# Performance work log

Measured on AMD Instinct MI355X. Metric: run time of the kernel, lower is better.

## Reference

```python
import jax, jax.numpy as jnp
import numpy as np

MPPI_ITER = 6
HORIZON = 18
NUM_SAMPLES = 65536
ACTION_DIM = 4
NUM_ELITES = 64
STD = 0.5
MOMENTUM = 0.1
TEMPERATURE = 1.0


def setup_inputs() -> dict:
    key = jax.random.key(0)
    k1, k2, k3 = jax.random.split(key, 3)
    pi_actions = jax.random.normal(k1, (HORIZON, NUM_SAMPLES, ACTION_DIM), dtype=jnp.float32)
    noise = jax.random.normal(k2, (MPPI_ITER, HORIZON, NUM_SAMPLES, ACTION_DIM), dtype=jnp.float32)
    target = jax.random.normal(k3, (HORIZON, ACTION_DIM), dtype=jnp.float32)
    return {"pi_actions": pi_actions, "noise": noise, "target": target}


def _value(actions, target):
    # Surrogate for methods.estimate_value: quadratic trajectory cost.
    # actions: [H, N, A], target: [H, A] -> value: [N]
    return -jnp.sum((actions - target[:, None, :]) ** 2, axis=(0, 2))


def reference(pi_actions, noise, target):
    H, N, A = pi_actions.shape
    mean = pi_actions[:, 0, :]                      # [H, A]
    std = jnp.ones((H, A), dtype=pi_actions.dtype)  # [H, A]
    elite_actions = pi_actions[:, :NUM_ELITES, :]
    for i in range(MPPI_ITER):
        # sample CEM trajectories around (mean, std), clamp to action bounds
        cem_actions = jnp.clip(
            mean[:, None, :] + STD * std[:, None, :] * noise[i], -4.0, 4.0
        )                                                      # [H, N, A]
        actions = jnp.concatenate([pi_actions, cem_actions], axis=1)  # [H, 2N, A]
        value = _value(actions, target)                        # [2N]
        elite_value, elite_idxs = jax.lax.top_k(value, NUM_ELITES)    # [E]
        elite_actions = actions[:, elite_idxs, :]              # [H, E, A]
        # exp-weighted reweighting (faithful double normalization of `score`)
        max_value = jnp.max(elite_value)
        score = jnp.exp(TEMPERATURE * (elite_value - max_value))
        score = score / jnp.sum(score)
        ssum = jnp.sum(score)
        _mean = jnp.sum(score[None, :, None] * elite_actions, axis=1) / (ssum + 1e-9)
        _std = jnp.sqrt(
            jnp.sum(score[None, :, None] * (elite_actions - _mean[:, None, :]) ** 2, axis=1)
            / (ssum + 1e-9)
        )
        # faithful reproduction of clamp_(horizon, 2): min=18 > max=2 -> pins to 2
        _std = jnp.clip(_std, float(H), 2.0)
        mean = MOMENTUM * mean + (1.0 - MOMENTUM) * _mean
        std = _std
    a = elite_actions[:, 0, :]  # best elite action sequence [H, A]
    return a
```

## Files before the change

### kernel.cpp

```cpp
#include <hip/hip_runtime.h>
#include <math.h>

#define H 18
#define NS 65536
#define AD 4
#define HAD 72
#define ITERS 6
#define DELTA 16.0f
#define SCAP 2048
#define NCH 2048

__device__ __forceinline__ unsigned encf(float f) {
    unsigned u = __float_as_uint(f);
    return (u & 0x80000000u) ? ~u : (u | 0x80000000u);
}
__device__ __forceinline__ float decf(unsigned u) {
    return __uint_as_float((u & 0x80000000u) ? (u & 0x7FFFFFFFu) : ~u);
}
__device__ __forceinline__ float clamp4f(float x) { return fminf(fmaxf(x, -4.0f), 4.0f); }
__device__ __forceinline__ unsigned long long packkey(float v, unsigned idx) {
    return ((unsigned long long)encf(v) << 32) | (unsigned long long)(~idx);
}

#define QH0(q) ((q) == 0 ? 0 : (q) == 1 ? 5 : (q) == 2 ? 10 : 14)
#define QCN(q) ((q) < 2 ? 5 : 4)

__global__ void __launch_bounds__(256, 4) k_value0(
        const float4* __restrict__ pi4, const float4* __restrict__ nz4,
        const float* __restrict__ target, float* __restrict__ meanarr,
        float* __restrict__ v_pi, float* __restrict__ wmax_pi,
        float* __restrict__ v_c0, float* __restrict__ wmax_c0) {
    __shared__ float tgt[HAD], mnL[HAD];
    __shared__ float smaxc[4], smaxp[4];
    const int tid = threadIdx.x, wg = blockIdx.x;
    const int lane = tid & 63, wid = tid >> 6;
    const int q = lane >> 4, s = lane & 15;
    const int n = wg * 64 + wid * 16 + s;
    const int h0 = QH0(q), cnt = QCN(q);

    float4 xs0 = nz4[(size_t)(h0 + 0) * NS + n];
    float4 xs1 = nz4[(size_t)(h0 + 1) * NS + n];
    float4 xs2 = nz4[(size_t)(h0 + 2) * NS + n];
    float4 xs3 = nz4[(size_t)(h0 + 3) * NS + n];
    const int h4 = (h0 + 4 > 17) ? 17 : h0 + 4;
    float4 xs4 = nz4[(size_t)h4 * NS + n];
    float4 ps0 = pi4[(size_t)(h0 + 0) * NS + n];
    float4 ps1 = pi4[(size_t)(h0 + 1) * NS + n];
    float4 ps2 = pi4[(size_t)(h0 + 2) * NS + n];
    float4 ps3 = pi4[(size_t)(h0 + 3) * NS + n];
    float4 ps4 = pi4[(size_t)h4 * NS + n];

    if (tid < HAD) {
        tgt[tid] = target[tid];
        float m0 = ((const float*)pi4)[(size_t)(tid >> 2) * NS * AD + (tid & 3)];
        mnL[tid] = m0;
        meanarr[tid] = m0;
    }
    __syncthreads();

    const float w4 = (cnt == 5) ? 1.0f : 0.0f;
    float a2 = 0.f, p2 = 0.f;
    {
        float c; int h;
        h = h0 + 0;
        c = clamp4f(mnL[h*4+0] + 0.5f*xs0.x) - tgt[h*4+0]; a2 += c*c;
        c = clamp4f(mnL[h*4+1] + 0.5f*xs0.y) - tgt[h*4+1]; a2 += c*c;
        c = clamp4f(mnL[h*4+2] + 0.5f*xs0.z) - tgt[h*4+2]; a2 += c*c;
        c = clamp4f(mnL[h*4+3] + 0.5f*xs0.w) - tgt[h*4+3]; a2 += c*c;
        c = ps0.x - tgt[h*4+0]; p2 += c*c;  c = ps0.y - tgt[h*4+1]; p2 += c*c;
        c = ps0.z - tgt[h*4+2]; p2 += c*c;  c = ps0.w - tgt[h*4+3]; p2 += c*c;
        h = h0 + 1;
        c = clamp4f(mnL[h*4+0] + 0.5f*xs1.x) - tgt[h*4+0]; a2 += c*c;
        c = clamp4f(mnL[h*4+1] + 0.5f*xs1.y) - tgt[h*4+1]; a2 += c*c;
        c = clamp4f(mnL[h*4+2] + 0.5f*xs1.z) - tgt[h*4+2]; a2 += c*c;
        c = clamp4f(mnL[h*4+3] + 0.5f*xs1.w) - tgt[h*4+3]; a2 += c*c;
        c = ps1.x - tgt[h*4+0]; p2 += c*c;  c = ps1.y - tgt[h*4+1]; p2 += c*c;
        c = ps1.z - tgt[h*4+2]; p2 += c*c;  c = ps1.w - tgt[h*4+3]; p2 += c*c;
        h = h0 + 2;
        c = clamp4f(mnL[h*4+0] + 0.5f*xs2.x) - tgt[h*4+0]; a2 += c*c;
        c = clamp4f(mnL[h*4+1] + 0.5f*xs2.y) - tgt[h*4+1]; a2 += c*c;
        c = clamp4f(mnL[h*4+2] + 0.5f*xs2.z) - tgt[h*4+2]; a2 += c*c;
        c = clamp4f(mnL[h*4+3] + 0.5f*xs2.w) - tgt[h*4+3]; a2 += c*c;
        c = ps2.x - tgt[h*4+0]; p2 += c*c;  c = ps2.y - tgt[h*4+1]; p2 += c*c;
        c = ps2.z - tgt[h*4+2]; p2 += c*c;  c = ps2.w - tgt[h*4+3]; p2 += c*c;
        h = h0 + 3;
        c = clamp4f(mnL[h*4+0] + 0.5f*xs3.x) - tgt[h*4+0]; a2 += c*c;
        c = clamp4f(mnL[h*4+1] + 0.5f*xs3.y) - tgt[h*4+1]; a2 += c*c;
        c = clamp4f(mnL[h*4+2] + 0.5f*xs3.z) - tgt[h*4+2]; a2 += c*c;
        c = clamp4f(mnL[h*4+3] + 0.5f*xs3.w) - tgt[h*4+3]; a2 += c*c;
        c = ps3.x - tgt[h*4+0]; p2 += c*c;  c = ps3.y - tgt[h*4+1]; p2 += c*c;
        c = ps3.z - tgt[h*4+2]; p2 += c*c;  c = ps3.w - tgt[h*4+3]; p2 += c*c;
        h = h4;
        c = clamp4f(mnL[h*4+0] + 0.5f*xs4.x) - tgt[h*4+0]; a2 += w4*c*c;
        c = clamp4f(mnL[h*4+1] + 0.5f*xs4.y) - tgt[h*4+1]; a2 += w4*c*c;
        c = clamp4f(mnL[h*4+2] + 0.5f*xs4.z) - tgt[h*4+2]; a2 += w4*c*c;
        c = clamp4f(mnL[h*4+3] + 0.5f*xs4.w) - tgt[h*4+3]; a2 += w4*c*c;
        c = ps4.x - tgt[h*4+0]; p2 += w4*c*c;  c = ps4.y - tgt[h*4+1]; p2 += w4*c*c;
        c = ps4.z - tgt[h*4+2]; p2 += w4*c*c;  c = ps4.w - tgt[h*4+3]; p2 += w4*c*c;
    }
    a2 += __shfl_xor(a2, 16);  a2 += __shfl_xor(a2, 32);
    p2 += __shfl_xor(p2, 16);  p2 += __shfl_xor(p2, 32);
    const float vc = -a2, vp = -p2;
    if (lane < 16) { v_c0[n] = vc; v_pi[n] = vp; }
    float mc = vc, mp = vp;
#pragma unroll
    for (int off = 8; off; off >>= 1) {
        mc = fmaxf(mc, __shfl_xor(mc, off));
        mp = fmaxf(mp, __shfl_xor(mp, off));
    }
    if (lane == 0) { smaxc[wid] = mc; smaxp[wid] = mp; }
    __syncthreads();
    if (tid == 0) {
        wmax_c0[wg * 2 + 0] = fmaxf(smaxc[0], smaxc[1]);
        wmax_c0[wg * 2 + 1] = fmaxf(smaxc[2], smaxc[3]);
        wmax_pi[wg * 2 + 0] = fmaxf(smaxp[0], smaxp[1]);
        wmax_pi[wg * 2 + 1] = fmaxf(smaxp[2], smaxp[3]);
    }
}

__global__ void __launch_bounds__(256, 4) k_value(
        const float4* __restrict__ nz4, const float* __restrict__ target,
        const float* __restrict__ meanarr_i,
        float* __restrict__ v_out, float* __restrict__ wmax_out) {
    __shared__ float tgt[HAD], mnL[HAD];
    __shared__ float smax[4];
    const int tid = threadIdx.x, wg = blockIdx.x;
    const int lane = tid & 63, wid = tid >> 6;
    const int q = lane >> 4, s = lane & 15;
    const int n = wg * 64 + wid * 16 + s;
    const int h0 = QH0(q), cnt = QCN(q);

    float4 xs0 = nz4[(size_t)(h0 + 0) * NS + n];
    float4 xs1 = nz4[(size_t)(h0 + 1) * NS + n];
    float4 xs2 = nz4[(size_t)(h0 + 2) * NS + n];
    float4 xs3 = nz4[(size_t)(h0 + 3) * NS + n];
    const int h4 = (h0 + 4 > 17) ? 17 : h0 + 4;
    float4 xs4 = nz4[(size_t)h4 * NS + n];

    if (tid < HAD) { tgt[tid] = target[tid]; mnL[tid] = meanarr_i[tid]; }
    __syncthreads();

    const float w4 = (cnt == 5) ? 1.0f : 0.0f;
    float a2 = 0.f;
    {
        float c; int h;
        h = h0 + 0;
        c = clamp4f(mnL[h*4+0] + xs0.x) - tgt[h*4+0]; a2 += c*c;
        c = clamp4f(mnL[h*4+1] + xs0.y) - tgt[h*4+1]; a2 += c*c;
        c = clamp4f(mnL[h*4+2] + xs0.z) - tgt[h*4+2]; a2 += c*c;
        c = clamp4f(mnL[h*4+3] + xs0.w) - tgt[h*4+3]; a2 += c*c;
        h = h0 + 1;
        c = clamp4f(mnL[h*4+0] + xs1.x) - tgt[h*4+0]; a2 += c*c;
        c = clamp4f(mnL[h*4+1] + xs1.y) - tgt[h*4+1]; a2 += c*c;
        c = clamp4f(mnL[h*4+2] + xs1.z) - tgt[h*4+2]; a2 += c*c;
        c = clamp4f(mnL[h*4+3] + xs1.w) - tgt[h*4+3]; a2 += c*c;
        h = h0 + 2;
        c = clamp4f(mnL[h*4+0] + xs2.x) - tgt[h*4+0]; a2 += c*c;
        c = clamp4f(mnL[h*4+1] + xs2.y) - tgt[h*4+1]; a2 += c*c;
        c = clamp4f(mnL[h*4+2] + xs2.z) - tgt[h*4+2]; a2 += c*c;
        c = clamp4f(mnL[h*4+3] + xs2.w) - tgt[h*4+3]; a2 += c*c;
        h = h0 + 3;
        c = clamp4f(mnL[h*4+0] + xs3.x) - tgt[h*4+0]; a2 += c*c;
        c = clamp4f(mnL[h*4+1] + xs3.y) - tgt[h*4+1]; a2 += c*c;
        c = clamp4f(mnL[h*4+2] + xs3.z) - tgt[h*4+2]; a2 += c*c;
        c = clamp4f(mnL[h*4+3] + xs3.w) - tgt[h*4+3]; a2 += c*c;
        h = h4;
        c = clamp4f(mnL[h*4+0] + xs4.x) - tgt[h*4+0]; a2 += w4*c*c;
        c = clamp4f(mnL[h*4+1] + xs4.y) - tgt[h*4+1]; a2 += w4*c*c;
        c = clamp4f(mnL[h*4+2] + xs4.z) - tgt[h*4+2]; a2 += w4*c*c;
        c = clamp4f(mnL[h*4+3] + xs4.w) - tgt[h*4+3]; a2 += w4*c*c;
    }
    a2 += __shfl_xor(a2, 16);  a2 += __shfl_xor(a2, 32);
    const float vc = -a2;
    if (lane < 16) v_out[n] = vc;
    float m = vc;
#pragma unroll
    for (int off = 8; off; off >>= 1) m = fmaxf(m, __shfl_xor(m, off));
    if (lane == 0) smax[wid] = m;
    __syncthreads();
    if (tid == 0) {
        wmax_out[wg * 2 + 0] = fmaxf(smax[0], smax[1]);
        wmax_out[wg * 2 + 1] = fmaxf(smax[2], smax[3]);
    }
}

__global__ void __launch_bounds__(1024) k_reduce(
        const float* __restrict__ pi, const float* __restrict__ noise_i,
        float* __restrict__ meanarr,
        const float* __restrict__ wmax_pi, const float* __restrict__ v_pi,
        const float* __restrict__ wmax_c, const float* __restrict__ v_c,
        float* __restrict__ out, int iter, int is_last) {
    __shared__ unsigned long long skey[SCAP];
    __shared__ unsigned long long top[64];
    __shared__ unsigned long long redk[16];
    __shared__ float buf[64 * 76];
    __shared__ float w64[64];
    __shared__ float mprev[HAD];
    __shared__ float redf[16];
    __shared__ unsigned s_fcnt;
    __shared__ float s_S, s_gmax;
    const int tid = threadIdx.x, lane = tid & 63, wid = tid >> 6;

    if (tid < HAD) mprev[tid] = meanarr[iter * HAD + tid];
    if (tid == 0) s_fcnt = 0u;
    __syncthreads();

    {
        float g = fmaxf(fmaxf(wmax_pi[tid], wmax_pi[tid + 1024]),
                        fmaxf(wmax_c[tid], wmax_c[tid + 1024]));
        for (int off = 32; off; off >>= 1) g = fmaxf(g, __shfl_xor(g, off));
        if (lane == 0) redf[wid] = g;
        __syncthreads();
        if (tid == 0) {
            float x = redf[0];
            for (int q = 1; q < 16; ++q) x = fmaxf(x, redf[q]);
            s_gmax = x;
        }
        __syncthreads();
    }
    const float gmax = s_gmax, thr = gmax - DELTA;

#pragma unroll
    for (int r = 0; r < 2; ++r) {
        const int c = tid + r * 1024;
        if (wmax_pi[c] >= thr) {
            const float4* v4 = (const float4*)v_pi + c * 8;
            for (int q = 0; q < 8; ++q) {
                float4 x = v4[q];
                float vv[4] = {x.x, x.y, x.z, x.w};
#pragma unroll
                for (int c2 = 0; c2 < 4; ++c2)
                    if (vv[c2] >= thr) {
                        unsigned p = atomicAdd(&s_fcnt, 1u);
                        if (p < SCAP) skey[p] = packkey(vv[c2], (unsigned)(c * 32 + q * 4 + c2));
                    }
            }
        }
        if (wmax_c[c] >= thr) {
            const float4* v4 = (const float4*)v_c + c * 8;
            for (int q = 0; q < 8; ++q) {
                float4 x = v4[q];
                float vv[4] = {x.x, x.y, x.z, x.w};
#pragma unroll
                for (int c2 = 0; c2 < 4; ++c2)
                    if (vv[c2] >= thr) {
                        unsigned p = atomicAdd(&s_fcnt, 1u);
                        if (p < SCAP) skey[p] = packkey(vv[c2], (unsigned)(NS + c * 32 + q * 4 + c2));
                    }
            }
        }
    }
    __syncthreads();
    unsigned fc = s_fcnt; if (fc > SCAP) fc = SCAP;
    const float pscale = (iter == 0) ? 0.5f : 1.0f;

    if (is_last) {
        unsigned long long bk = 0ull;
        for (unsigned k = tid; k < fc; k += 1024) if (skey[k] > bk) bk = skey[k];
        for (int off = 32; off; off >>= 1) {
            unsigned long long ok = __shfl_xor(bk, off);
            if (ok > bk) bk = ok;
        }
        if (lane == 0) redk[wid] = bk;
        __syncthreads();
        if (tid == 0) {
            unsigned long long b = redk[0];
            for (int q = 1; q < 16; ++q) if (redk[q] > b) b = redk[q];
            redk[0] = b;
        }
        __syncthreads();
        const unsigned idx = (unsigned)~(unsigned)(redk[0] & 0xFFFFFFFFull);
        if (tid < HAD) {
            const int h = tid >> 2, aa = tid & 3;
            float o;
            if (idx < NS) o = pi[(size_t)h * NS * AD + (size_t)idx * AD + aa];
            else o = clamp4f(mprev[tid] + pscale * noise_i[(size_t)h * NS * AD + (size_t)(idx - NS) * AD + aa]);
            out[tid] = o;
        }
        return;
    }

    for (unsigned i = tid; i < fc; i += 1024) {
        unsigned long long k = skey[i];
        unsigned r = 0;
        for (unsigned j = 0; j < fc; ++j) r += (skey[j] > k) ? 1u : 0u;
        if (r < 64u) top[r] = k;
    }
    if (fc < 64u)
        for (unsigned r = fc + tid; r < 64u; r += 1024) top[r] = 0ull;
    __syncthreads();
    const int E = (fc < 64u) ? (int)fc : 64;

    if (tid < 64) {
        float we = (tid < E) ? expf(decf((unsigned)(top[tid] >> 32)) - gmax) : 0.0f;
        w64[tid] = we;
        float s = we;
        for (int off = 32; off; off >>= 1) s += __shfl_xor(s, off);
        if (tid == 0) s_S = s;
    }
    __syncthreads();
    const float invS = 1.0f / (s_S * (1.0f + 1e-9f));

    const float4* pi4 = (const float4*)pi;
    const float4* nz4 = (const float4*)noise_i;
    for (int el = tid; el < 64 * H; el += 1024) {
        const int e = el / H, h = el - e * H;
        float ax = 0.f, ay = 0.f, az = 0.f, aw = 0.f;
        if (e < E) {
            const unsigned idx = (unsigned)~(unsigned)(top[e] & 0xFFFFFFFFull);
            float4 a;
            if (idx < NS) {
                a = pi4[(size_t)h * NS + idx];
            } else {
                float4 nz = nz4[(size_t)h * NS + (idx - NS)];
                a.x = clamp4f(mprev[h*4+0] + pscale * nz.x);
                a.y = clamp4f(mprev[h*4+1] + pscale * nz.y);
                a.z = clamp4f(mprev[h*4+2] + pscale * nz.z);
                a.w = clamp4f(mprev[h*4+3] + pscale * nz.w);
            }
            const float we = w64[e];
            ax = we * a.x; ay = we * a.y; az = we * a.z; aw = we * a.w;
        }
        buf[e * 76 + h * 4 + 0] = ax;
        buf[e * 76 + h * 4 + 1] = ay;
        buf[e * 76 + h * 4 + 2] = az;
        buf[e * 76 + h * 4 + 3] = aw;
    }
    __syncthreads();
    if (tid < HAD) {
        float s = 0.f;
#pragma unroll 8
        for (int e = 0; e < 64; ++e) s += buf[e * 76 + tid];
        meanarr[(iter + 1) * HAD + tid] = 0.1f * mprev[tid] + 0.9f * (s * invS);
    }
}

extern "C" void kernel_launch(void* const* d_in, const int* in_sizes, int n_in,
                              void* d_out, int out_size, void* d_ws, size_t ws_size,
                              hipStream_t stream) {
    const float* pi     = (const float*)d_in[0];
    const float* noise  = (const float*)d_in[1];
    const float* target = (const float*)d_in[2];
    float* out = (float*)d_out;

    float* ws = (float*)d_ws;
    float* meanarr = ws;
    float* wmax_pi = ws + 1024;
    float* wmax_c  = wmax_pi + NCH;
    float* v_pi    = wmax_c + 6 * NCH;
    float* v_c     = v_pi + NS;

    k_value0<<<1024, 256, 0, stream>>>((const float4*)pi, (const float4*)noise,
                                       target, meanarr, v_pi, wmax_pi, v_c, wmax_c);
    for (int i = 0; i < ITERS - 1; ++i) {
        const float* nzi = noise + (size_t)i * H * NS * AD;
        k_reduce<<<1, 1024, 0, stream>>>(pi, nzi, meanarr, wmax_pi, v_pi,
                                         wmax_c + (size_t)i * NCH,
                                         v_c + (size_t)i * NS, out, i, 0);
        const float* nzn = noise + (size_t)(i + 1) * H * NS * AD;
        k_value<<<1024, 256, 0, stream>>>((const float4*)nzn, target,
                                          meanarr + (size_t)(i + 1) * HAD,
                                          v_c + (size_t)(i + 1) * NS,
                                          wmax_c + (size_t)(i + 1) * NCH);
    }
    k_reduce<<<1, 1024, 0, stream>>>(pi, noise + (size_t)5 * H * NS * AD, meanarr,
                                     wmax_pi, v_pi,
                                     wmax_c + (size_t)5 * NCH,
                                     v_c + (size_t)5 * NS, out, 5, 1);
}
```

Before: 139.9 us.

## Fuse elite reduction into value kernel with redundant per-block top-k

```diff
diff --git a/kernel.cpp b/kernel.cpp
--- a/kernel.cpp
+++ b/kernel.cpp
@@ -118,27 +118,149 @@
     }
 }
 
-__global__ void __launch_bounds__(256, 4) k_value(
-        const float4* __restrict__ nz4, const float* __restrict__ target,
-        const float* __restrict__ meanarr_i,
-        float* __restrict__ v_out, float* __restrict__ wmax_out) {
-    __shared__ float tgt[HAD], mnL[HAD];
+__global__ void __launch_bounds__(256, 2) k_fused(
+        const float* __restrict__ pi, const float* __restrict__ noise,
+        const float* __restrict__ target, float* __restrict__ meanarr,
+        const float* __restrict__ wmax_pi, const float* __restrict__ v_pi,
+        const float* __restrict__ wmax_prev, const float* __restrict__ v_prev,
+        float* __restrict__ v_out, float* __restrict__ wmax_out, int iter) {
+    __shared__ unsigned long long skey[SCAP];
+    __shared__ unsigned long long top[64];
+    __shared__ float buf[64 * 76];
+    __shared__ float w64[64];
+    __shared__ float tgt[HAD], mnL[HAD], mprev[HAD];
+    __shared__ float redf[4];
+    __shared__ unsigned s_fcnt;
+    __shared__ float s_S, s_gmax;
     __shared__ float smax[4];
+
     const int tid = threadIdx.x, wg = blockIdx.x;
     const int lane = tid & 63, wid = tid >> 6;
-    const int q = lane >> 4, s = lane & 15;
-    const int n = wg * 64 + wid * 16 + s;
+
+    if (tid < HAD) {
+        tgt[tid] = target[tid];
+        mprev[tid] = meanarr[(size_t)(iter - 1) * HAD + tid];
+    }
+    if (tid == 0) s_fcnt = 0u;
+    __syncthreads();
+
+    {
+        float g = -INFINITY;
+#pragma unroll
+        for (int r = 0; r < 8; ++r) {
+            const int k = tid + r * 256;
+            g = fmaxf(g, fmaxf(wmax_pi[k], wmax_prev[k]));
+        }
+        for (int off = 32; off; off >>= 1) g = fmaxf(g, __shfl_xor(g, off));
+        if (lane == 0) redf[wid] = g;
+        __syncthreads();
+        if (tid == 0)
+            s_gmax = fmaxf(fmaxf(redf[0], redf[1]), fmaxf(redf[2], redf[3]));
+        __syncthreads();
+    }
+    const float gmax = s_gmax, thr = gmax - DELTA;
+
+#pragma unroll
+    for (int r = 0; r < 8; ++r) {
+        const int c = tid + r * 256;
+        if (wmax_pi[c] >= thr) {
+            const float4* v4 = (const float4*)v_pi + c * 8;
+            for (int q = 0; q < 8; ++q) {
+                float4 x = v4[q];
+                float vv[4] = {x.x, x.y, x.z, x.w};
+#pragma unroll
+                for (int c2 = 0; c2 < 4; ++c2)
+                    if (vv[c2] >= thr) {
+                        unsigned p = atomicAdd(&s_fcnt, 1u);
+                        if (p < SCAP) skey[p] = packkey(vv[c2], (unsigned)(c * 32 + q * 4 + c2));
+                    }
+            }
+        }
+        if (wmax_prev[c] >= thr) {
+            const float4* v4 = (const float4*)v_prev + c * 8;
+            for (int q = 0; q < 8; ++q) {
+                float4 x = v4[q];
+                float vv[4] = {x.x, x.y, x.z, x.w};
+#pragma unroll
+                for (int c2 = 0; c2 < 4; ++c2)
+                    if (vv[c2] >= thr) {
+                        unsigned p = atomicAdd(&s_fcnt, 1u);
+                        if (p < SCAP) skey[p] = packkey(vv[c2], (unsigned)(NS + c * 32 + q * 4 + c2));
+                    }
+            }
+        }
+    }
+    __syncthreads();
+    unsigned fc = s_fcnt; if (fc > SCAP) fc = SCAP;
+
+    for (unsigned i = tid; i < fc; i += 256) {
+        unsigned long long k = skey[i];
+        unsigned r = 0;
+        for (unsigned j = 0; j < fc; ++j) r += (skey[j] > k) ? 1u : 0u;
+        if (r < 64u) top[r] = k;
+    }
+    if (fc < 64u)
+        for (unsigned r = fc + tid; r < 64u; r += 256) top[r] = 0ull;
+    __syncthreads();
+    const int E = (fc < 64u) ? (int)fc : 64;
+
+    if (tid < 64) {
+        float we = (tid < E) ? expf(decf((unsigned)(top[tid] >> 32)) - gmax) : 0.0f;
+        w64[tid] = we;
+        float s = we;
+        for (int off = 32; off; off >>= 1) s += __shfl_xor(s, off);
+        if (tid == 0) s_S = s;
+    }
+    __syncthreads();
+    const float invS = 1.0f / (s_S * (1.0f + 1e-9f));
+
+    const float pscale = (iter == 1) ? 0.5f : 1.0f;
+    const float4* pi4 = (const float4*)pi;
+    const float4* nzp4 = (const float4*)(noise + (size_t)(iter - 1) * H * NS * AD);
+    for (int el = tid; el < 64 * H; el += 256) {
+        const int e = el / H, h = el - e * H;
+        float ax = 0.f, ay = 0.f, az = 0.f, aw = 0.f;
+        if (e < E) {
+            const unsigned idx = (unsigned)~(unsigned)(top[e] & 0xFFFFFFFFull);
+            float4 a;
+            if (idx < NS) {
+                a = pi4[(size_t)h * NS + idx];
+            } else {
+                float4 nz = nzp4[(size_t)h * NS + (idx - NS)];
+                a.x = clamp4f(mprev[h*4+0] + pscale * nz.x);
+                a.y = clamp4f(mprev[h*4+1] + pscale * nz.y);
+                a.z = clamp4f(mprev[h*4+2] + pscale * nz.z);
+                a.w = clamp4f(mprev[h*4+3] + pscale * nz.w);
+            }
+            const float we = w64[e];
+            ax = we * a.x; ay = we * a.y; az = we * a.z; aw = we * a.w;
+        }
+        buf[e * 76 + h * 4 + 0] = ax;
+        buf[e * 76 + h * 4 + 1] = ay;
+        buf[e * 76 + h * 4 + 2] = az;
+        buf[e * 76 + h * 4 + 3] = aw;
+    }
+    __syncthreads();
+    if (tid < HAD) {
+        float s = 0.f;
+#pragma unroll 8
+        for (int e = 0; e < 64; ++e) s += buf[e * 76 + tid];
+        float nm = 0.1f * mprev[tid] + 0.9f * (s * invS);
+        mnL[tid] = nm;
+        meanarr[(size_t)iter * HAD + tid] = nm;
+    }
+    __syncthreads();
+
+    const int q = lane >> 4, s2 = lane & 15;
+    const int n = wg * 64 + wid * 16 + s2;
     const int h0 = QH0(q), cnt = QCN(q);
-
+    const float4* nz4 = (const float4*)(noise + (size_t)iter * H * NS * AD);
     float4 xs0 = nz4[(size_t)(h0 + 0) * NS + n];
     float4 xs1 = nz4[(size_t)(h0 + 1) * NS + n];
     float4 xs2 = nz4[(size_t)(h0 + 2) * NS + n];
     float4 xs3 = nz4[(size_t)(h0 + 3) * NS + n];
     const int h4 = (h0 + 4 > 17) ? 17 : h0 + 4;
     float4 xs4 = nz4[(size_t)h4 * NS + n];
-
-    if (tid < HAD) { tgt[tid] = target[tid]; mnL[tid] = meanarr_i[tid]; }
-    __syncthreads();
 
     const float w4 = (cnt == 5) ? 1.0f : 0.0f;
     float a2 = 0.f;
@@ -184,27 +306,19 @@
     }
 }
 
-__global__ void __launch_bounds__(1024) k_reduce(
+__global__ void __launch_bounds__(1024) k_final(
         const float* __restrict__ pi, const float* __restrict__ noise_i,
-        float* __restrict__ meanarr,
+        const float* __restrict__ meanarr,
         const float* __restrict__ wmax_pi, const float* __restrict__ v_pi,
         const float* __restrict__ wmax_c, const float* __restrict__ v_c,
-        float* __restrict__ out, int iter, int is_last) {
-    __shared__ unsigned long long skey[SCAP];
-    __shared__ unsigned long long top[64];
+        float* __restrict__ out) {
     __shared__ unsigned long long redk[16];
-    __shared__ float buf[64 * 76];
-    __shared__ float w64[64];
     __shared__ float mprev[HAD];
     __shared__ float redf[16];
-    __shared__ unsigned s_fcnt;
-    __shared__ float s_S, s_gmax;
+    __shared__ float s_gmax;
     const int tid = threadIdx.x, lane = tid & 63, wid = tid >> 6;
 
-    if (tid < HAD) mprev[tid] = meanarr[iter * HAD + tid];
-    if (tid == 0) s_fcnt = 0u;
-    __syncthreads();
-
+    if (tid < HAD) mprev[tid] = meanarr[(size_t)5 * HAD + tid];
     {
         float g = fmaxf(fmaxf(wmax_pi[tid], wmax_pi[tid + 1024]),
                         fmaxf(wmax_c[tid], wmax_c[tid + 1024]));
@@ -218,120 +332,57 @@
         }
         __syncthreads();
     }
-    const float gmax = s_gmax, thr = gmax - DELTA;
-
+    const float gmax = s_gmax;
+    unsigned long long bk = 0ull;
 #pragma unroll
     for (int r = 0; r < 2; ++r) {
         const int c = tid + r * 1024;
-        if (wmax_pi[c] >= thr) {
+        if (wmax_pi[c] >= gmax) {
             const float4* v4 = (const float4*)v_pi + c * 8;
             for (int q = 0; q < 8; ++q) {
                 float4 x = v4[q];
                 float vv[4] = {x.x, x.y, x.z, x.w};
 #pragma unroll
                 for (int c2 = 0; c2 < 4; ++c2)
-                    if (vv[c2] >= thr) {
-                        unsigned p = atomicAdd(&s_fcnt, 1u);
-                        if (p < SCAP) skey[p] = packkey(vv[c2], (unsigned)(c * 32 + q * 4 + c2));
+                    if (vv[c2] >= gmax) {
+                        unsigned long long key = packkey(vv[c2], (unsigned)(c * 32 + q * 4 + c2));
+                        if (key > bk) bk = key;
                     }
             }
         }
-        if (wmax_c[c] >= thr) {
+        if (wmax_c[c] >= gmax) {
             const float4* v4 = (const float4*)v_c + c * 8;
             for (int q = 0; q < 8; ++q) {
                 float4 x = v4[q];
                 float vv[4] = {x.x, x.y, x.z, x.w};
 #pragma unroll
                 for (int c2 = 0; c2 < 4; ++c2)
-                    if (vv[c2] >= thr) {
-                        unsigned p = atomicAdd(&s_fcnt, 1u);
-                        if (p < SCAP) skey[p] = packkey(vv[c2], (unsigned)(NS + c * 32 + q * 4 + c2));
+                    if (vv[c2] >= gmax) {
+                        unsigned long long key = packkey(vv[c2], (unsigned)(NS + c * 32 + q * 4 + c2));
+                        if (key > bk) bk = key;
                     }
             }
         }
     }
-    __syncthreads();
-    unsigned fc = s_fcnt; if (fc > SCAP) fc = SCAP;
-    const float pscale = (iter == 0) ? 0.5f : 1.0f;
-
-    if (is_last) {
-        unsigned long long bk = 0ull;
-        for (unsigned k = tid; k < fc; k += 1024) if (skey[k] > bk) bk = skey[k];
-        for (int off = 32; off; off >>= 1) {
-            unsigned long long ok = __shfl_xor(bk, off);
-            if (ok > bk) bk = ok;
-        }
-        if (lane == 0) redk[wid] = bk;
-        __syncthreads();
-        if (tid == 0) {
-            unsigned long long b = redk[0];
-            for (int q = 1; q < 16; ++q) if (redk[q] > b) b = redk[q];
-            redk[0] = b;
-        }
-        __syncthreads();
-        const unsigned idx = (unsigned)~(unsigned)(redk[0] & 0xFFFFFFFFull);
-        if (tid < HAD) {
-            const int h = tid >> 2, aa = tid & 3;
-            float o;
-            if (idx < NS) o = pi[(size_t)h * NS * AD + (size_t)idx * AD + aa];
-            else o = clamp4f(mprev[tid] + pscale * noise_i[(size_t)h * NS * AD + (size_t)(idx - NS) * AD + aa]);
-            out[tid] = o;
-        }
-        return;
-    }
-
-    for (unsigned i = tid; i < fc; i += 1024) {
-        unsigned long long k = skey[i];
-        unsigned r = 0;
-        for (unsigned j = 0; j < fc; ++j) r += (skey[j] > k) ? 1u : 0u;
-        if (r < 64u) top[r] = k;
-    }
-    if (fc < 64u)
-        for (unsigned r = fc + tid; r < 64u; r += 1024) top[r] = 0ull;
-    __syncthreads();
-    const int E = (fc < 64u) ? (int)fc : 64;
-
-    if (tid < 64) {
-        float we = (tid < E) ? expf(decf((unsigned)(top[tid] >> 32)) - gmax) : 0.0f;
-        w64[tid] = we;
-        float s = we;
-        for (int off = 32; off; off >>= 1) s += __shfl_xor(s, off);
-        if (tid == 0) s_S = s;
-    }
-    __syncthreads();
-    const float invS = 1.0f / (s_S * (1.0f + 1e-9f));
-
-    const float4* pi4 = (const float4*)pi;
-    const float4* nz4 = (const float4*)noise_i;
-    for (int el = tid; el < 64 * H; el += 1024) {
-        const int e = el / H, h = el - e * H;
-        float ax = 0.f, ay = 0.f, az = 0.f, aw = 0.f;
-        if (e < E) {
-            const unsigned idx = (unsigned)~(unsigned)(top[e] & 0xFFFFFFFFull);
-            float4 a;
-            if (idx < NS) {
-                a = pi4[(size_t)h * NS + idx];
-            } else {
-                float4 nz = nz4[(size_t)h * NS + (idx - NS)];
-                a.x = clamp4f(mprev[h*4+0] + pscale * nz.x);
-                a.y = clamp4f(mprev[h*4+1] + pscale * nz.y);
-                a.z = clamp4f(mprev[h*4+2] + pscale * nz.z);
-                a.w = clamp4f(mprev[h*4+3] + pscale * nz.w);
-            }
-            const float we = w64[e];
-            ax = we * a.x; ay = we * a.y; az = we * a.z; aw = we * a.w;
-        }
-        buf[e * 76 + h * 4 + 0] = ax;
-        buf[e * 76 + h * 4 + 1] = ay;
-        buf[e * 76 + h * 4 + 2] = az;
-        buf[e * 76 + h * 4 + 3] = aw;
-    }
-    __syncthreads();
+    for (int off = 32; off; off >>= 1) {
+        unsigned long long ok = __shfl_xor(bk, off);
+        if (ok > bk) bk = ok;
+    }
+    if (lane == 0) redk[wid] = bk;
+    __syncthreads();
+    if (tid == 0) {
+        unsigned long long b = redk[0];
+        for (int q = 1; q < 16; ++q) if (redk[q] > b) b = redk[q];
+        redk[0] = b;
+    }
+    __syncthreads();
+    const unsigned idx = (unsigned)~(unsigned)(redk[0] & 0xFFFFFFFFull);
     if (tid < HAD) {
-        float s = 0.f;
-#pragma unroll 8
-        for (int e = 0; e < 64; ++e) s += buf[e * 76 + tid];
-        meanarr[(iter + 1) * HAD + tid] = 0.1f * mprev[tid] + 0.9f * (s * invS);
+        const int h = tid >> 2, aa = tid & 3;
+        float o;
+        if (idx < NS) o = pi[(size_t)h * NS * AD + (size_t)idx * AD + aa];
+        else o = clamp4f(mprev[tid] + noise_i[(size_t)h * NS * AD + (size_t)(idx - NS) * AD + aa]);
+        out[tid] = o;
     }
 }
 
@@ -352,19 +403,15 @@
 
     k_value0<<<1024, 256, 0, stream>>>((const float4*)pi, (const float4*)noise,
                                        target, meanarr, v_pi, wmax_pi, v_c, wmax_c);
-    for (int i = 0; i < ITERS - 1; ++i) {
-        const float* nzi = noise + (size_t)i * H * NS * AD;
-        k_reduce<<<1, 1024, 0, stream>>>(pi, nzi, meanarr, wmax_pi, v_pi,
-                                         wmax_c + (size_t)i * NCH,
-                                         v_c + (size_t)i * NS, out, i, 0);
-        const float* nzn = noise + (size_t)(i + 1) * H * NS * AD;
-        k_value<<<1024, 256, 0, stream>>>((const float4*)nzn, target,
-                                          meanarr + (size_t)(i + 1) * HAD,
-                                          v_c + (size_t)(i + 1) * NS,
-                                          wmax_c + (size_t)(i + 1) * NCH);
-    }
-    k_reduce<<<1, 1024, 0, stream>>>(pi, noise + (size_t)5 * H * NS * AD, meanarr,
-                                     wmax_pi, v_pi,
-                                     wmax_c + (size_t)5 * NCH,
-                                     v_c + (size_t)5 * NS, out, 5, 1);
-}
+    for (int i = 1; i < ITERS; ++i)
+        k_fused<<<1024, 256, 0, stream>>>(pi, noise, target, meanarr,
+                                          wmax_pi, v_pi,
+                                          wmax_c + (size_t)(i - 1) * NCH,
+                                          v_c + (size_t)(i - 1) * NS,
+                                          v_c + (size_t)i * NS,
+                                          wmax_c + (size_t)i * NCH, i);
+    k_final<<<1, 1024, 0, stream>>>(pi, noise + (size_t)5 * H * NS * AD, meanarr,
+                                    wmax_pi, v_pi,
+                                    wmax_c + (size_t)5 * NCH,
+                                    v_c + (size_t)5 * NS, out);
+}
```

New measurement: 248.1 us. +77.3%, slower.
